# Performance work log

Hardware: AMD Instinct MI355X
Metric: run time of the kernel (lower is better)

The kernel has to match this reference:

```python
import jax, jax.numpy as jnp
import numpy as np

B, NE, DE = 4096, 64, 96
NA, NACT = 8, 16
DH, NH, OD = 256, 4, 64
HD = DH // NH


def setup_inputs() -> dict:
    key = jax.random.key(0)
    ks = jax.random.split(key, 16)
    s = 0.02
    entities = jax.random.normal(ks[0], (B, NE, DE), jnp.float32)
    entity_mask = jax.random.randint(ks[1], (B, NE), 0, 2, jnp.int32)
    obs_mask = jax.random.randint(ks[2], (B, NE, NE), 0, 2, jnp.int32)
    act_ids = jax.random.randint(ks[3], (B, NA), 0, NACT)
    actions_onehot = jax.nn.one_hot(act_ids, NACT, dtype=jnp.float32)
    return {
        "entities": entities,
        "entity_mask": entity_mask,
        "obs_mask": obs_mask,
        "actions_onehot": actions_onehot,
        "We": jax.random.normal(ks[4], (DE, DH), jnp.float32) * s,
        "be": jnp.zeros((DH,), jnp.float32),
        "Wa": jax.random.normal(ks[5], (NACT, DH), jnp.float32) * s,
        "Win": jax.random.normal(ks[6], (DH, 3 * DH), jnp.float32) * s,
        "Wout": jax.random.normal(ks[7], (DH, DH), jnp.float32) * s,
        "bout": jnp.zeros((DH,), jnp.float32),
        "Wm1": jax.random.normal(ks[8], (DH, DH), jnp.float32) * s,
        "bm1": jnp.zeros((DH,), jnp.float32),
        "Wm2": jax.random.normal(ks[9], (DH, OD), jnp.float32) * s,
        "bm2": jnp.zeros((OD,), jnp.float32),
        "Wl1": jax.random.normal(ks[10], (DH, DH), jnp.float32) * s,
        "bl1": jnp.zeros((DH,), jnp.float32),
        "Wl2": jax.random.normal(ks[11], (DH, OD), jnp.float32) * s,
        "bl2": jnp.zeros((OD,), jnp.float32),
    }


def reference(entities, entity_mask, obs_mask, actions_onehot,
              We, be, Wa, Win, Wout, bout,
              Wm1, bm1, Wm2, bm2, Wl1, bl1, Wl2, bl2):
    # entity encode + action embed, scattered into first NA entity slots
    he = entities @ We + be                      # [B, NE, DH]
    ha = actions_onehot @ Wa                     # [B, NA, DH]
    ha_pad = jnp.zeros_like(he).at[:, :NA].set(ha)
    x = jax.nn.relu(he + ha_pad)                 # [B, NE, DH]

    # multi-head attention: NA agent queries attend to NE entities
    qkv = x @ Win                                # [B, NE, 3*DH]
    q, k, v = jnp.split(qkv, 3, axis=-1)
    q = q[:, :NA].reshape(B, NA, NH, HD)
    k = k.reshape(B, NE, NH, HD)
    v = v.reshape(B, NE, NH, HD)
    logits = jnp.einsum('bqhd,bkhd->bhqk', q, k) / jnp.sqrt(jnp.float32(HD))
    pre = obs_mask[:, :NA, :NE].astype(bool)[:, None, :, :]  # [B,1,NA,NE]
    logits = jnp.where(pre, -jnp.inf, logits)
    w = jax.nn.softmax(logits, axis=-1)
    w = jnp.where(jnp.isnan(w), 0.0, w)          # fully-masked rows -> 0
    attn = jnp.einsum('bhqk,bkhd->bqhd', w, v).reshape(B, NA, DH)
    attn = attn @ Wout + bout
    post = entity_mask[:, :NA].astype(bool)[..., None]  # [B, NA, 1]
    hidden = jax.nn.relu(jnp.where(post, 0.0, attn))

    mean = jax.nn.relu(hidden @ Wm1 + bm1) @ Wm2 + bm2
    logvar = jnp.clip(jax.nn.relu(hidden @ Wl1 + bl1) @ Wl2 + bl2, -10.0, 0.0)
    return mean, logvar
```

## Files before the change

kernel.cpp:

```cpp
#include <hip/hip_runtime.h>
#include <hip/hip_bf16.h>
#include <math.h>

typedef __attribute__((ext_vector_type(8))) short short8;
typedef __attribute__((ext_vector_type(4))) float f32x4;
typedef __attribute__((ext_vector_type(2))) unsigned int uint2v;

#define DEVINL static __device__ __forceinline__


static constexpr int WE_OFF  = 0;
static constexpr int MQK_OFF = 24576;
static constexpr int WV_OFF  = 286720;
static constexpr int WO_OFF  = 352256;
static constexpr int WM1_OFF = 417792;
static constexpr int WM2_OFF = 483328;
static constexpr int WL1_OFF = 499712;
static constexpr int WL2_OFF = 565248;
static constexpr int ATTN_OFF = 581632;

static constexpr int XOFF   = 0;
static constexpr int VTOFF  = 32768;
static constexpr int EOFF   = 65536;
static constexpr int ACTOFF = 77824;
static constexpr int LDS_F  = 81920;

static constexpr int B_AT = 0;
static constexpr int B_H  = 32768;
static constexpr int B_EM = 65536;
static constexpr int LDS_B = 65792;

DEVINL unsigned short f2bf(float f) {
  union { float f; unsigned u; } x; x.f = f;
  unsigned r = x.u + 0x7fffu + ((x.u >> 16) & 1u);
  return (unsigned short)(r >> 16);
}

DEVINL f32x4 mfma(short8 a, short8 b, f32x4 c) {
  return __builtin_amdgcn_mfma_f32_16x16x32_bf16(a, b, c, 0, 0, 0);
}

DEVINL short8 ldfrag(const unsigned short* wf, int off, int nt, int kt, int nkt, int lane) {
  return *(const short8*)(wf + off + ((nt * nkt + kt) << 9) + (lane << 3));
}

__global__ __launch_bounds__(512) void prep_frag(
    const float* We, const float* Win, const float* Wout, const float* Wm1,
    const float* Wm2, const float* Wl1, const float* Wl2, unsigned short* wf) {
  const int m = blockIdx.y;
  const int Ks[7]  = {96, 256, 256, 256, 256, 256, 256};
  const int Ns[7]  = {256, 256, 256, 256, 64, 256, 64};
  const int ld_[7] = {256, 768, 256, 256, 64, 256, 64};
  const int co_[7] = {0, 512, 0, 0, 0, 0, 0};
  const int off[7] = {WE_OFF, WV_OFF, WO_OFF, WM1_OFF, WM2_OFF, WL1_OFF, WL2_OFF};
  const float* S[7] = {We, Win, Wout, Wm1, Wm2, Wl1, Wl2};
  const int K = Ks[m], N = Ns[m], nkt = K >> 5;
  const int fid = blockIdx.x * 512 + threadIdx.x;
  if (fid >= (N >> 4) * nkt * 64) return;
  const int lane = fid & 63;
  const int kt = (fid >> 6) % nkt;
  const int nt = fid / (nkt << 6);
  const int row0 = kt * 32 + ((lane >> 4) << 3);
  const int col = nt * 16 + (lane & 15);
  const float* sp = S[m] + (long)row0 * ld_[m] + co_[m] + col;
  const int ld = ld_[m];
  short8 s;
#pragma unroll
  for (int j = 0; j < 8; ++j) s[j] = (short)f2bf(sp[j * ld]);
  *(short8*)(wf + off[m] + fid * 8) = s;
}

__global__ __launch_bounds__(1024) void prep_mqk(const float* __restrict__ Win,
                                                 unsigned short* __restrict__ wf) {
  __shared__ char smq[65536];
  const int h = blockIdx.x;
  const int tid = threadIdx.x;
  const int w = tid >> 6, lane = tid & 63, g = lane >> 4, c = lane & 15;
  {
    const int d = tid >> 2, hd0 = (tid & 3) * 16;
    const int sw = (d & 7) << 4;
#pragma unroll
    for (int mat = 0; mat < 2; ++mat) {
      const float* srcp = Win + (long)d * 768 + mat * 256 + h * 64 + hd0;
      short8 s0, s1;
#pragma unroll
      for (int j = 0; j < 8; ++j) s0[j] = (short)f2bf(srcp[j]);
#pragma unroll
      for (int j = 0; j < 8; ++j) s1[j] = (short)f2bf(srcp[8 + j]);
      char* base = smq + mat * 32768 + d * 128;
      *(short8*)(base + ((hd0 * 2) ^ sw)) = s0;
      *(short8*)(base + ((hd0 * 2 + 16) ^ sw)) = s1;
    }
  }
  __syncthreads();
#pragma unroll 4
  for (int mt = 0; mt < 16; ++mt) {
    f32x4 acc = {0.f, 0.f, 0.f, 0.f};
#pragma unroll
    for (int kt = 0; kt < 2; ++kt) {
      const int ra = mt * 16 + c;
      short8 a = *(const short8*)(smq + ra * 128 + ((kt * 64 + g * 16) ^ ((ra & 7) << 4)));
      const int rb = w * 16 + c;
      short8 b = *(const short8*)(smq + 32768 + rb * 128 + ((kt * 64 + g * 16) ^ ((rb & 7) << 4)));
      acc = mfma(a, b, acc);
    }
#pragma unroll
    for (int r = 0; r < 4; ++r) {
      const int d1 = mt * 16 + g * 4 + r;
      wf[MQK_OFF + h * 65536 + ((w * 8 + (d1 >> 5)) << 9) +
         ((((d1 >> 3) & 3) << 4) + c) * 8 + (d1 & 7)] = f2bf(acc[r]);
    }
  }
}

__global__ __launch_bounds__(512, 4) void front_kernel(
    const float* __restrict__ entities, const int* __restrict__ obs_mask,
    const float* __restrict__ acts, const float* __restrict__ Wa,
    const float* __restrict__ be, const unsigned short* __restrict__ wf,
    unsigned short* __restrict__ attn_g) {
  extern __shared__ char sm[];
  const int tid = threadIdx.x;
  const int w = tid >> 6, lane = tid & 63;
  const int g = lane >> 4, c = lane & 15;
  const long ig = blockIdx.x;

  {
    const int row = tid >> 3, seg = tid & 7;
    const float* src = entities + ig * 6144 + row * 96 + seg * 12;
    const int ebase = EOFF + row * 192;
    const int sw = (row & 3) << 4;
#pragma unroll
    for (int p = 0; p < 3; ++p) {
      float4 f = *(const float4*)(src + p * 4);
      uint2v u;
      u.x = f2bf(f.x) | ((unsigned)f2bf(f.y) << 16);
      u.y = f2bf(f.z) | ((unsigned)f2bf(f.w) << 16);
      *(uint2v*)(sm + ebase + ((seg * 24 + p * 8) ^ sw)) = u;
    }
    if (tid < 8) {
      const float* oh = acts + (ig * 8 + tid) * 16;
      int id = 0;
#pragma unroll
      for (int a = 0; a < 16; ++a) if (oh[a] > 0.5f) id = a;
      ((int*)(sm + ACTOFF))[tid] = id;
    }
  }
  __syncthreads();

  {
    f32x4 acc[4][2] = {};
#pragma unroll
    for (int kt = 0; kt < 3; ++kt) {
      short8 b0 = ldfrag(wf, WE_OFF, 2 * w, kt, 3, lane);
      short8 b1 = ldfrag(wf, WE_OFF, 2 * w + 1, kt, 3, lane);
#pragma unroll
      for (int mt = 0; mt < 4; ++mt) {
        const int row = mt * 16 + c;
        short8 a = *(const short8*)(sm + EOFF + row * 192 +
                                    ((kt * 64 + g * 16) ^ ((row & 3) << 4)));
        acc[mt][0] = mfma(a, b0, acc[mt][0]);
        acc[mt][1] = mfma(a, b1, acc[mt][1]);
      }
    }
#pragma unroll
    for (int n = 0; n < 2; ++n) {
      const int col = (2 * w + n) * 16 + c;
      const float bev = be[col];
#pragma unroll
      for (int mt = 0; mt < 4; ++mt)
#pragma unroll
        for (int r = 0; r < 4; ++r) {
          const int row = mt * 16 + g * 4 + r;
          float v = acc[mt][n][r] + bev;
          if (row < 8) {
            int id = ((const int*)(sm + ACTOFF))[row];
            v += Wa[id * 256 + col];
          }
          v = fmaxf(v, 0.f);
          *(unsigned short*)(sm + XOFF + row * 512 +
                             ((col * 2) ^ ((row & 7) << 4))) = f2bf(v);
        }
    }
  }
  __syncthreads();

  {
    const int h = w >> 1;
    f32x4 ta[8] = {};
#pragma unroll
    for (int kt = 0; kt < 8; ++kt) {
      short8 a = *(const short8*)(sm + XOFF + (c & 7) * 512 +
                                  ((kt * 64 + g * 16) ^ ((c & 7) << 4)));
#pragma unroll
      for (int n = 0; n < 8; ++n) {
        short8 b = ldfrag(wf, MQK_OFF + h * 65536, (w & 1) * 8 + n, kt, 8, lane);
        ta[n] = mfma(a, b, ta[n]);
      }
    }
    if (g < 2) {
#pragma unroll
      for (int n = 0; n < 8; ++n) {
        const int nt = (w & 1) * 8 + n;
#pragma unroll
        for (int r = 0; r < 4; ++r) {
          const int q = g * 4 + r;
          const int col = nt * 16 + c;
          *(unsigned short*)(sm + EOFF + h * 4096 + q * 512 +
                             ((col * 2) ^ (q << 4))) = f2bf(ta[n][r]);
        }
      }
    }
  }
  __syncthreads();

  {
    float wvals[4][4];
    const int h = w;
    if (w < 4) {
      f32x4 lac[4] = {};
#pragma unroll
      for (int kt = 0; kt < 8; ++kt) {
        short8 a = *(const short8*)(sm + EOFF + h * 4096 + (c & 7) * 512 +
                                    ((kt * 64 + g * 16) ^ ((c & 7) << 4)));
#pragma unroll
        for (int nt = 0; nt < 4; ++nt) {
          const int key = nt * 16 + c;
          short8 b = *(const short8*)(sm + XOFF + key * 512 +
                                      ((kt * 64 + g * 16) ^ ((key & 7) << 4)));
          lac[nt] = mfma(a, b, lac[nt]);
        }
      }
      if (g < 2) {
        const int* obs = obs_mask + ig * 4096;
#pragma unroll
        for (int r = 0; r < 4; ++r) {
          const int qi = g * 4 + r;
          float vals[4];
#pragma unroll
          for (int nt = 0; nt < 4; ++nt) {
            int msk = obs[qi * 64 + nt * 16 + c];
            vals[nt] = msk ? -INFINITY : lac[nt][r] * 0.125f;
          }
          float mx = fmaxf(fmaxf(vals[0], vals[1]), fmaxf(vals[2], vals[3]));
#pragma unroll
          for (int d = 1; d < 16; d <<= 1) mx = fmaxf(mx, __shfl_xor(mx, d, 64));
          float s = 0.f;
#pragma unroll
          for (int nt = 0; nt < 4; ++nt) {
            float e = (mx == -INFINITY) ? 0.f : __expf(vals[nt] - mx);
            vals[nt] = e; s += e;
          }
#pragma unroll
          for (int d = 1; d < 16; d <<= 1) s += __shfl_xor(s, d, 64);
          const float inv = (s > 0.f) ? 1.f / s : 0.f;
#pragma unroll
          for (int nt = 0; nt < 4; ++nt) wvals[r][nt] = vals[nt] * inv;
        }
      }
    }
    __syncthreads();
    if (w < 4 && g < 2) {
#pragma unroll
      for (int r = 0; r < 4; ++r) {
        const int qi = g * 4 + r;
#pragma unroll
        for (int nt = 0; nt < 4; ++nt) {
          const int key = nt * 16 + c;
          *(unsigned short*)(sm + EOFF + (h * 8 + qi) * 128 +
                             ((key * 2) ^ (qi << 4))) = f2bf(wvals[r][nt]);
        }
      }
    }
  }

  {
    f32x4 acc[4][2] = {};
#pragma unroll
    for (int kt = 0; kt < 8; ++kt) {
      short8 b0 = ldfrag(wf, WV_OFF, 2 * w, kt, 8, lane);
      short8 b1 = ldfrag(wf, WV_OFF, 2 * w + 1, kt, 8, lane);
#pragma unroll
      for (int mt = 0; mt < 4; ++mt) {
        const int row = mt * 16 + c;
        short8 a = *(const short8*)(sm + XOFF + row * 512 +
                                    ((kt * 64 + g * 16) ^ ((row & 7) << 4)));
        acc[mt][0] = mfma(a, b0, acc[mt][0]);
        acc[mt][1] = mfma(a, b1, acc[mt][1]);
      }
    }
#pragma unroll
    for (int n = 0; n < 2; ++n) {
      const int col = (2 * w + n) * 16 + c;
#pragma unroll
      for (int mt = 0; mt < 4; ++mt) {
        unsigned long long pk = 0;
#pragma unroll
        for (int r = 0; r < 4; ++r)
          pk |= (unsigned long long)f2bf(acc[mt][n][r]) << (16 * r);
        *(unsigned long long*)(sm + VTOFF + col * 128 +
                               ((mt * 32 + g * 8) ^ ((col & 7) << 4))) = pk;
      }
    }
  }
  __syncthreads();

  {
    f32x4 aac[2] = {};
#pragma unroll
    for (int e = 0; e < 2; ++e) {
      const int tt = w * 2 + e, h = tt >> 2, n2 = tt & 3;
#pragma unroll
      for (int kt = 0; kt < 2; ++kt) {
        short8 a = *(const short8*)(sm + EOFF + h * 1024 + (c & 7) * 128 +
                                    ((kt * 64 + g * 16) ^ ((c & 7) << 4)));
        const int vrow = h * 64 + n2 * 16 + c;
        short8 b = *(const short8*)(sm + VTOFF + vrow * 128 +
                                    ((kt * 64 + g * 16) ^ ((vrow & 7) << 4)));
        aac[e] = mfma(a, b, aac[e]);
      }
    }
    if (g < 2) {
#pragma unroll
      for (int e = 0; e < 2; ++e) {
        const int tt = w * 2 + e, h = tt >> 2, n2 = tt & 3;
#pragma unroll
        for (int r = 0; r < 4; ++r) {
          const int q = g * 4 + r;
          const int col = h * 64 + n2 * 16 + c;
          attn_g[(ig * 8 + q) * 256 + (col ^ (q << 3))] = f2bf(aac[e][r]);
        }
      }
    }
  }
}

__global__ __launch_bounds__(512, 4) void back_kernel(
    const int* __restrict__ entity_mask, const float* __restrict__ bout,
    const float* __restrict__ bm1, const float* __restrict__ bm2,
    const float* __restrict__ bl1, const float* __restrict__ bl2,
    const unsigned short* __restrict__ wf, const unsigned short* __restrict__ attn_g,
    float* __restrict__ out) {
  extern __shared__ char sm[];
  const int tid = threadIdx.x;
  const int w = tid >> 6, lane = tid & 63;
  const int g = lane >> 4, c = lane & 15;
  const long blk = blockIdx.x;

  {
    const uint4* src = (const uint4*)(attn_g + blk * 16384);
#pragma unroll
    for (int itr = 0; itr < 4; ++itr)
      *(uint4*)(sm + B_AT + itr * 8192 + tid * 16) = src[itr * 512 + tid];
    if (tid < 64)
      ((int*)(sm + B_EM))[tid] = entity_mask[(blk * 8 + (tid >> 3)) * 64 + (tid & 7)];
  }
  __syncthreads();

  {
    f32x4 acc[4][2] = {};
#pragma unroll
    for (int kt = 0; kt < 8; ++kt) {
      short8 b0 = ldfrag(wf, WO_OFF, 2 * w, kt, 8, lane);
      short8 b1 = ldfrag(wf, WO_OFF, 2 * w + 1, kt, 8, lane);
#pragma unroll
      for (int mt = 0; mt < 4; ++mt) {
        const int row = mt * 16 + c;
        short8 a = *(const short8*)(sm + B_AT + row * 512 +
                                    ((kt * 64 + g * 16) ^ ((row & 7) << 4)));
        acc[mt][0] = mfma(a, b0, acc[mt][0]);
        acc[mt][1] = mfma(a, b1, acc[mt][1]);
      }
    }
#pragma unroll
    for (int n = 0; n < 2; ++n) {
      const int col = (2 * w + n) * 16 + c;
      const float bo = bout[col];
#pragma unroll
      for (int mt = 0; mt < 4; ++mt)
#pragma unroll
        for (int r = 0; r < 4; ++r) {
          const int row = mt * 16 + g * 4 + r;
          const int em = ((const int*)(sm + B_EM))[row];
          float v = acc[mt][n][r] + bo;
          v = em ? 0.f : fmaxf(v, 0.f);
          *(unsigned short*)(sm + B_H + row * 512 +
                             ((col * 2) ^ ((row & 7) << 4))) = f2bf(v);
        }
    }
  }
  __syncthreads();

  {
    f32x4 acc[4][2] = {};
#pragma unroll
    for (int kt = 0; kt < 8; ++kt) {
      short8 b0 = ldfrag(wf, WM1_OFF, 2 * w, kt, 8, lane);
      short8 b1 = ldfrag(wf, WM1_OFF, 2 * w + 1, kt, 8, lane);
#pragma unroll
      for (int mt = 0; mt < 4; ++mt) {
        const int row = mt * 16 + c;
        short8 a = *(const short8*)(sm + B_H + row * 512 +
                                    ((kt * 64 + g * 16) ^ ((row & 7) << 4)));
        acc[mt][0] = mfma(a, b0, acc[mt][0]);
        acc[mt][1] = mfma(a, b1, acc[mt][1]);
      }
    }
#pragma unroll
    for (int n = 0; n < 2; ++n) {
      const int col = (2 * w + n) * 16 + c;
      const float bv = bm1[col];
#pragma unroll
      for (int mt = 0; mt < 4; ++mt)
#pragma unroll
        for (int r = 0; r < 4; ++r) {
          const int row = mt * 16 + g * 4 + r;
          float v = fmaxf(acc[mt][n][r] + bv, 0.f);
          *(unsigned short*)(sm + B_AT + row * 512 +
                             ((col * 2) ^ ((row & 7) << 4))) = f2bf(v);
        }
    }
  }
  __syncthreads();

  {
    const int mh = w >> 2, nt = w & 3;
    f32x4 acc[2] = {};
#pragma unroll
    for (int kt = 0; kt < 8; ++kt) {
      short8 b = ldfrag(wf, WM2_OFF, nt, kt, 8, lane);
#pragma unroll
      for (int m2 = 0; m2 < 2; ++m2) {
        const int row = (mh * 2 + m2) * 16 + c;
        short8 a = *(const short8*)(sm + B_AT + row * 512 +
                                    ((kt * 64 + g * 16) ^ ((row & 7) << 4)));
        acc[m2] = mfma(a, b, acc[m2]);
      }
    }
    const float bv = bm2[nt * 16 + c];
#pragma unroll
    for (int m2 = 0; m2 < 2; ++m2)
#pragma unroll
      for (int r = 0; r < 4; ++r) {
        const int row = (mh * 2 + m2) * 16 + g * 4 + r;
        out[(blk * 8 + (row >> 3)) * 512 + (row & 7) * 64 + nt * 16 + c] = acc[m2][r] + bv;
      }
  }
  __syncthreads();

  {
    f32x4 acc[4][2] = {};
#pragma unroll
    for (int kt = 0; kt < 8; ++kt) {
      short8 b0 = ldfrag(wf, WL1_OFF, 2 * w, kt, 8, lane);
      short8 b1 = ldfrag(wf, WL1_OFF, 2 * w + 1, kt, 8, lane);
#pragma unroll
      for (int mt = 0; mt < 4; ++mt) {
        const int row = mt * 16 + c;
        short8 a = *(const short8*)(sm + B_H + row * 512 +
                                    ((kt * 64 + g * 16) ^ ((row & 7) << 4)));
        acc[mt][0] = mfma(a, b0, acc[mt][0]);
        acc[mt][1] = mfma(a, b1, acc[mt][1]);
      }
    }
#pragma unroll
    for (int n = 0; n < 2; ++n) {
      const int col = (2 * w + n) * 16 + c;
      const float bv = bl1[col];
#pragma unroll
      for (int mt = 0; mt < 4; ++mt)
#pragma unroll
        for (int r = 0; r < 4; ++r) {
          const int row = mt * 16 + g * 4 + r;
          float v = fmaxf(acc[mt][n][r] + bv, 0.f);
          *(unsigned short*)(sm + B_AT + row * 512 +
                             ((col * 2) ^ ((row & 7) << 4))) = f2bf(v);
        }
    }
  }
  __syncthreads();

  {
    const int mh = w >> 2, nt = w & 3;
    f32x4 acc[2] = {};
#pragma unroll
    for (int kt = 0; kt < 8; ++kt) {
      short8 b = ldfrag(wf, WL2_OFF, nt, kt, 8, lane);
#pragma unroll
      for (int m2 = 0; m2 < 2; ++m2) {
        const int row = (mh * 2 + m2) * 16 + c;
        short8 a = *(const short8*)(sm + B_AT + row * 512 +
                                    ((kt * 64 + g * 16) ^ ((row & 7) << 4)));
        acc[m2] = mfma(a, b, acc[m2]);
      }
    }
    const float bv = bl2[nt * 16 + c];
#pragma unroll
    for (int m2 = 0; m2 < 2; ++m2)
#pragma unroll
      for (int r = 0; r < 4; ++r) {
        const int row = (mh * 2 + m2) * 16 + g * 4 + r;
        float v = acc[m2][r] + bv;
        v = fminf(fmaxf(v, -10.f), 0.f);
        out[2097152 + (blk * 8 + (row >> 3)) * 512 + (row & 7) * 64 + nt * 16 + c] = v;
      }
  }
}

extern "C" void kernel_launch(void* const* d_in, const int* in_sizes, int n_in,
                              void* d_out, int out_size, void* d_ws, size_t ws_size,
                              hipStream_t stream) {
  const float* entities    = (const float*)d_in[0];
  const int*   entity_mask = (const int*)d_in[1];
  const int*   obs_mask    = (const int*)d_in[2];
  const float* acts        = (const float*)d_in[3];
  const float* We   = (const float*)d_in[4];
  const float* be   = (const float*)d_in[5];
  const float* Wa   = (const float*)d_in[6];
  const float* Win  = (const float*)d_in[7];
  const float* Wout = (const float*)d_in[8];
  const float* bout = (const float*)d_in[9];
  const float* Wm1  = (const float*)d_in[10];
  const float* bm1  = (const float*)d_in[11];
  const float* Wm2  = (const float*)d_in[12];
  const float* bm2  = (const float*)d_in[13];
  const float* Wl1  = (const float*)d_in[14];
  const float* bl1  = (const float*)d_in[15];
  const float* Wl2  = (const float*)d_in[16];
  const float* bl2  = (const float*)d_in[17];
  unsigned short* wf = (unsigned short*)d_ws;
  unsigned short* attn_g = wf + ATTN_OFF;

  prep_frag<<<dim3(16, 7), 512, 0, stream>>>(We, Win, Wout, Wm1, Wm2, Wl1, Wl2, wf);
  prep_mqk<<<4, 1024, 0, stream>>>(Win, wf);

  hipFuncSetAttribute((const void*)front_kernel,
                      hipFuncAttributeMaxDynamicSharedMemorySize, LDS_F);
  hipFuncSetAttribute((const void*)back_kernel,
                      hipFuncAttributeMaxDynamicSharedMemorySize, LDS_B);

  front_kernel<<<4096, 512, LDS_F, stream>>>(entities, obs_mask, acts, Wa, be, wf, attn_g);
  back_kernel<<<512, 512, LDS_B, stream>>>(entity_mask, bout, bm1, bm2, bl1, bl2,
                                           wf, attn_g, (float*)d_out);
}
```

Measured before the change: 388.0 us.

## Replace precomputed Wq·Wkᵀ product with explicit Q projection then Kᵀ fold

Drops the prep kernel that folded Wq·Wkᵀ per head into a 256x256 matrix. The front kernel now computes Q = x·Wq for the 8 agent rows, then multiplies Q by a per-head transposed Wk to get q·Wkᵀ. This reads much less weight data per block (Wq plus Wkᵀ instead of four 256x256 folded matrices) at the cost of an extra LDS round-trip and barrier. It also prefetches the obs_mask values and Wa action rows into registers early, and switches bf16 conversion to the HIP intrinsic.

Result: faster. 337.3 us (-13.1%).

```diff
diff --git a/kernel.cpp b/kernel.cpp
--- a/kernel.cpp
+++ b/kernel.cpp
@@ -10,18 +10,20 @@
 
 
 static constexpr int WE_OFF  = 0;
-static constexpr int MQK_OFF = 24576;
-static constexpr int WV_OFF  = 286720;
-static constexpr int WO_OFF  = 352256;
-static constexpr int WM1_OFF = 417792;
-static constexpr int WM2_OFF = 483328;
-static constexpr int WL1_OFF = 499712;
-static constexpr int WL2_OFF = 565248;
-static constexpr int ATTN_OFF = 581632;
+static constexpr int WQ_OFF  = 24576;
+static constexpr int WKT_OFF = 90112;
+static constexpr int WV_OFF  = 155648;
+static constexpr int WO_OFF  = 221184;
+static constexpr int WM1_OFF = 286720;
+static constexpr int WM2_OFF = 352256;
+static constexpr int WL1_OFF = 368640;
+static constexpr int WL2_OFF = 434176;
+static constexpr int ATTN_OFF = 450560;
 
 static constexpr int XOFF   = 0;
 static constexpr int VTOFF  = 32768;
 static constexpr int EOFF   = 65536;
+static constexpr int QO     = 77824;
 static constexpr int ACTOFF = 77824;
 static constexpr int LDS_F  = 81920;
 
@@ -31,9 +33,8 @@
 static constexpr int LDS_B = 65792;
 
 DEVINL unsigned short f2bf(float f) {
-  union { float f; unsigned u; } x; x.f = f;
-  unsigned r = x.u + 0x7fffu + ((x.u >> 16) & 1u);
-  return (unsigned short)(r >> 16);
+  __hip_bfloat16 h = __float2bfloat16(f);
+  return __builtin_bit_cast(unsigned short, h);
 }
 
 DEVINL f32x4 mfma(short8 a, short8 b, f32x4 c) {
@@ -48,14 +49,28 @@
     const float* We, const float* Win, const float* Wout, const float* Wm1,
     const float* Wm2, const float* Wl1, const float* Wl2, unsigned short* wf) {
   const int m = blockIdx.y;
-  const int Ks[7]  = {96, 256, 256, 256, 256, 256, 256};
-  const int Ns[7]  = {256, 256, 256, 256, 64, 256, 64};
-  const int ld_[7] = {256, 768, 256, 256, 64, 256, 64};
-  const int co_[7] = {0, 512, 0, 0, 0, 0, 0};
-  const int off[7] = {WE_OFF, WV_OFF, WO_OFF, WM1_OFF, WM2_OFF, WL1_OFF, WL2_OFF};
-  const float* S[7] = {We, Win, Wout, Wm1, Wm2, Wl1, Wl2};
+  const int fid = blockIdx.x * 512 + threadIdx.x;
+  if (m == 2) {
+    if (fid >= 8192) return;
+    const int lane = fid & 63;
+    const int kt = (fid >> 6) & 1;
+    const int nt = (fid >> 7) & 15;
+    const int h  = fid >> 11;
+    const int d  = nt * 16 + (lane & 15);
+    const float* sp = Win + (long)d * 768 + 256 + h * 64 + kt * 32 + ((lane >> 4) << 3);
+    short8 s;
+#pragma unroll
+    for (int j = 0; j < 8; ++j) s[j] = (short)f2bf(sp[j]);
+    *(short8*)(wf + WKT_OFF + fid * 8) = s;
+    return;
+  }
+  const int Ks[9]  = {96, 256, 0, 256, 256, 256, 256, 256, 256};
+  const int Ns[9]  = {256, 256, 0, 256, 256, 256, 64, 256, 64};
+  const int ld_[9] = {256, 768, 0, 768, 256, 256, 64, 256, 64};
+  const int co_[9] = {0, 0, 0, 512, 0, 0, 0, 0, 0};
+  const int off[9] = {WE_OFF, WQ_OFF, 0, WV_OFF, WO_OFF, WM1_OFF, WM2_OFF, WL1_OFF, WL2_OFF};
+  const float* S[9] = {We, Win, Win, Win, Wout, Wm1, Wm2, Wl1, Wl2};
   const int K = Ks[m], N = Ns[m], nkt = K >> 5;
-  const int fid = blockIdx.x * 512 + threadIdx.x;
   if (fid >= (N >> 4) * nkt * 64) return;
   const int lane = fid & 63;
   const int kt = (fid >> 6) % nkt;
@@ -68,49 +83,6 @@
 #pragma unroll
   for (int j = 0; j < 8; ++j) s[j] = (short)f2bf(sp[j * ld]);
   *(short8*)(wf + off[m] + fid * 8) = s;
-}
-
-__global__ __launch_bounds__(1024) void prep_mqk(const float* __restrict__ Win,
-                                                 unsigned short* __restrict__ wf) {
-  __shared__ char smq[65536];
-  const int h = blockIdx.x;
-  const int tid = threadIdx.x;
-  const int w = tid >> 6, lane = tid & 63, g = lane >> 4, c = lane & 15;
-  {
-    const int d = tid >> 2, hd0 = (tid & 3) * 16;
-    const int sw = (d & 7) << 4;
-#pragma unroll
-    for (int mat = 0; mat < 2; ++mat) {
-      const float* srcp = Win + (long)d * 768 + mat * 256 + h * 64 + hd0;
-      short8 s0, s1;
-#pragma unroll
-      for (int j = 0; j < 8; ++j) s0[j] = (short)f2bf(srcp[j]);
-#pragma unroll
-      for (int j = 0; j < 8; ++j) s1[j] = (short)f2bf(srcp[8 + j]);
-      char* base = smq + mat * 32768 + d * 128;
-      *(short8*)(base + ((hd0 * 2) ^ sw)) = s0;
-      *(short8*)(base + ((hd0 * 2 + 16) ^ sw)) = s1;
-    }
-  }
-  __syncthreads();
-#pragma unroll 4
-  for (int mt = 0; mt < 16; ++mt) {
-    f32x4 acc = {0.f, 0.f, 0.f, 0.f};
-#pragma unroll
-    for (int kt = 0; kt < 2; ++kt) {
-      const int ra = mt * 16 + c;
-      short8 a = *(const short8*)(smq + ra * 128 + ((kt * 64 + g * 16) ^ ((ra & 7) << 4)));
-      const int rb = w * 16 + c;
-      short8 b = *(const short8*)(smq + 32768 + rb * 128 + ((kt * 64 + g * 16) ^ ((rb & 7) << 4)));
-      acc = mfma(a, b, acc);
-    }
-#pragma unroll
-    for (int r = 0; r < 4; ++r) {
-      const int d1 = mt * 16 + g * 4 + r;
-      wf[MQK_OFF + h * 65536 + ((w * 8 + (d1 >> 5)) << 9) +
-         ((((d1 >> 3) & 3) << 4) + c) * 8 + (d1 & 7)] = f2bf(acc[r]);
-    }
-  }
 }
 
 __global__ __launch_bounds__(512, 4) void front_kernel(
@@ -124,6 +96,16 @@
   const int g = lane >> 4, c = lane & 15;
   const long ig = blockIdx.x;
 
+  int obsv[16];
+  if (w < 4 && g < 2) {
+    const int* obs = obs_mask + ig * 4096;
+#pragma unroll
+    for (int r = 0; r < 4; ++r)
+#pragma unroll
+      for (int nt = 0; nt < 4; ++nt)
+        obsv[r * 4 + nt] = obs[(g * 4 + r) * 64 + nt * 16 + c];
+  }
+
   {
     const int row = tid >> 3, seg = tid & 7;
     const float* src = entities + ig * 6144 + row * 96 + seg * 12;
@@ -147,6 +129,16 @@
   }
   __syncthreads();
 
+  float wav[4][2] = {};
+  if (g < 2) {
+#pragma unroll
+    for (int r = 0; r < 4; ++r) {
+      const int id = ((const int*)(sm + ACTOFF))[g * 4 + r];
+      wav[r][0] = Wa[id * 256 + (2 * w) * 16 + c];
+      wav[r][1] = Wa[id * 256 + (2 * w + 1) * 16 + c];
+    }
+  }
+
   {
     f32x4 acc[4][2] = {};
 #pragma unroll
@@ -172,10 +164,7 @@
         for (int r = 0; r < 4; ++r) {
           const int row = mt * 16 + g * 4 + r;
           float v = acc[mt][n][r] + bev;
-          if (row < 8) {
-            int id = ((const int*)(sm + ACTOFF))[row];
-            v += Wa[id * 256 + col];
-          }
+          if (row < 8) v += wav[r][n];
           v = fmaxf(v, 0.f);
           *(unsigned short*)(sm + XOFF + row * 512 +
                              ((col * 2) ^ ((row & 7) << 4))) = f2bf(v);
@@ -185,28 +174,54 @@
   __syncthreads();
 
   {
-    const int h = w >> 1;
-    f32x4 ta[8] = {};
-#pragma unroll
-    for (int kt = 0; kt < 8; ++kt) {
+    f32x4 qa[2] = {};
+#pragma unroll
+    for (int kt = 0; kt < 8; ++kt) {
+      short8 b0 = ldfrag(wf, WQ_OFF, 2 * w, kt, 8, lane);
+      short8 b1 = ldfrag(wf, WQ_OFF, 2 * w + 1, kt, 8, lane);
       short8 a = *(const short8*)(sm + XOFF + (c & 7) * 512 +
                                   ((kt * 64 + g * 16) ^ ((c & 7) << 4)));
+      qa[0] = mfma(a, b0, qa[0]);
+      qa[1] = mfma(a, b1, qa[1]);
+    }
+    if (g < 2) {
+#pragma unroll
+      for (int n = 0; n < 2; ++n) {
+        const int col = (2 * w + n) * 16 + c;
+#pragma unroll
+        for (int r = 0; r < 4; ++r) {
+          const int qi = g * 4 + r;
+          *(unsigned short*)(sm + QO + qi * 512 +
+                             ((col * 2) ^ (qi << 4))) = f2bf(qa[n][r]);
+        }
+      }
+    }
+  }
+  __syncthreads();
+
+  {
+    const int h = w >> 1, hf = w & 1;
+    f32x4 ta[8] = {};
+#pragma unroll
+    for (int kt = 0; kt < 2; ++kt) {
+      short8 a = *(const short8*)(sm + QO + (c & 7) * 512 +
+                                  ((h * 128 + kt * 64 + g * 16) ^ ((c & 7) << 4)));
 #pragma unroll
       for (int n = 0; n < 8; ++n) {
-        short8 b = ldfrag(wf, MQK_OFF + h * 65536, (w & 1) * 8 + n, kt, 8, lane);
+        short8 b = ldfrag(wf, WKT_OFF, h * 16 + hf * 8 + n, kt, 2, lane);
         ta[n] = mfma(a, b, ta[n]);
       }
     }
+    __syncthreads();
     if (g < 2) {
 #pragma unroll
       for (int n = 0; n < 8; ++n) {
-        const int nt = (w & 1) * 8 + n;
-#pragma unroll
-        for (int r = 0; r < 4; ++r) {
-          const int q = g * 4 + r;
-          const int col = nt * 16 + c;
-          *(unsigned short*)(sm + EOFF + h * 4096 + q * 512 +
-                             ((col * 2) ^ (q << 4))) = f2bf(ta[n][r]);
+        const int col = (hf * 8 + n) * 16 + c;
+#pragma unroll
+        for (int r = 0; r < 4; ++r) {
+          const int qi = g * 4 + r;
+          *(unsigned short*)(sm + EOFF + h * 4096 + qi * 512 +
+                             ((col * 2) ^ (qi << 4))) = f2bf(ta[n][r]);
         }
       }
     }
@@ -231,16 +246,12 @@
         }
       }
       if (g < 2) {
-        const int* obs = obs_mask + ig * 4096;
-#pragma unroll
-        for (int r = 0; r < 4; ++r) {
-          const int qi = g * 4 + r;
+#pragma unroll
+        for (int r = 0; r < 4; ++r) {
           float vals[4];
 #pragma unroll
-          for (int nt = 0; nt < 4; ++nt) {
-            int msk = obs[qi * 64 + nt * 16 + c];
-            vals[nt] = msk ? -INFINITY : lac[nt][r] * 0.125f;
-          }
+          for (int nt = 0; nt < 4; ++nt)
+            vals[nt] = obsv[r * 4 + nt] ? -INFINITY : lac[nt][r] * 0.125f;
           float mx = fmaxf(fmaxf(vals[0], vals[1]), fmaxf(vals[2], vals[3]));
 #pragma unroll
           for (int d = 1; d < 16; d <<= 1) mx = fmaxf(mx, __shfl_xor(mx, d, 64));
@@ -530,8 +541,7 @@
   unsigned short* wf = (unsigned short*)d_ws;
   unsigned short* attn_g = wf + ATTN_OFF;
 
-  prep_frag<<<dim3(16, 7), 512, 0, stream>>>(We, Win, Wout, Wm1, Wm2, Wl1, Wl2, wf);
-  prep_mqk<<<4, 1024, 0, stream>>>(Win, wf);
+  prep_frag<<<dim3(16, 9), 512, 0, stream>>>(We, Win, Wout, Wm1, Wm2, Wl1, Wl2, wf);
 
   hipFuncSetAttribute((const void*)front_kernel,
                       hipFuncAttributeMaxDynamicSharedMemorySize, LDS_F);
```
